# Kernel tuning notes

Hardware: AMD Instinct MI355X
Metric: run time of the kernel (lower is better)

Reference implementation:

```python
import jax, jax.numpy as jnp
import numpy as np

B, N, C_IN, C_OUT, K = 2, 8192, 128, 128, 21  # K = num_neighbors + 1 (self)
EPS = 1e-5

def knn_idx(xyz, k):
    # xyz: [B,N,3] -> idx [B,N,k] of k nearest neighbors (self included)
    d2 = jnp.sum(xyz * xyz, axis=-1)  # [B,N]
    dist = d2[:, :, None] + d2[:, None, :] - 2.0 * jnp.einsum('bnd,bmd->bnm', xyz, xyz)
    _, idx = jax.lax.top_k(-dist, k)
    return idx

def group_points(pts, idx):
    # pts [B,N,D], idx [B,N,K] -> [B,N,K,D]
    return jax.vmap(lambda p, i: p[i])(pts, idx)

def group_feats(f, idx):
    # f [B,C,N], idx [B,N,K] -> [B,C,N,K]
    return jax.vmap(lambda ff, i: ff[:, i])(f, idx)

def conv_bn_relu(x, W, g, b, m, v):
    # 1x1 conv (bias=False) + BatchNorm (inference stats) + ReLU
    y = jnp.einsum('oc,bcnk->bonk', W, x)
    inv = g / jnp.sqrt(v + EPS)
    return jax.nn.relu(y * inv[None, :, None, None] + (b - m * inv)[None, :, None, None])

def setup_inputs():
    key = jax.random.key(0)
    ks = jax.random.split(key, 12)
    return {
        'xyz': jax.random.normal(ks[0], (B, N, 3), jnp.float32),
        'f': jax.random.normal(ks[1], (B, C_IN, N), jnp.float32),
        'W_geo': jax.random.normal(ks[2], (C_OUT, 6), jnp.float32) * 0.1,
        'g_geo': jax.random.uniform(ks[3], (C_OUT,), jnp.float32, 0.5, 1.5),
        'b_geo': jax.random.normal(ks[4], (C_OUT,), jnp.float32) * 0.1,
        'm_geo': jax.random.normal(ks[5], (C_OUT,), jnp.float32) * 0.1,
        'v_geo': jax.random.uniform(ks[6], (C_OUT,), jnp.float32, 0.5, 1.5),
        'W_feat': jax.random.normal(ks[7], (C_OUT, 2 * C_IN), jnp.float32) * 0.05,
        'g_feat': jax.random.uniform(ks[8], (C_OUT,), jnp.float32, 0.5, 1.5),
        'b_feat': jax.random.normal(ks[9], (C_OUT,), jnp.float32) * 0.1,
        'm_feat': jax.random.normal(ks[10], (C_OUT,), jnp.float32) * 0.1,
        'v_feat': jax.random.uniform(ks[11], (C_OUT,), jnp.float32, 0.5, 1.5),
    }

def reference(xyz, f, W_geo, g_geo, b_geo, m_geo, v_geo, W_feat, g_feat, b_feat, m_feat, v_feat):
    idx = knn_idx(xyz, K)                                   # [B,N,K]
    grouped_xyz = group_points(xyz, idx)                    # [B,N,K,3]
    xyz_diff = jnp.transpose(grouped_xyz - xyz[:, :, None, :], (0, 3, 1, 2))  # [B,3,N,K]
    center = jnp.broadcast_to(jnp.transpose(xyz, (0, 2, 1))[:, :, :, None], (B, 3, N, K))
    G_geo = jnp.concatenate([center, xyz_diff], axis=1)     # [B,6,N,K]
    grouped_f = group_feats(f, idx)                         # [B,C,N,K]
    center_f = jnp.broadcast_to(f[:, :, :, None], (B, C_IN, N, K))
    G_feat = jnp.concatenate([center_f, grouped_f - center_f], axis=1)  # [B,2C,N,K]
    G_geo = conv_bn_relu(G_geo, W_geo, g_geo, b_geo, m_geo, v_geo)      # [B,C_OUT,N,K]
    G_feat = conv_bn_relu(G_feat, W_feat, g_feat, b_feat, m_feat, v_feat)
    feature = jnp.concatenate([G_geo, G_feat], axis=1)      # [B,2*C_OUT,N,K]
    return jnp.max(feature, axis=-1)                        # [B,2*C_OUT,N]
```

## Files before the change

### kernel.cpp

```cpp
#include <hip/hip_runtime.h>

typedef unsigned int u32;
typedef unsigned long long u64;
typedef unsigned short u16;

#define DEV __device__ __forceinline__

DEV u16 f2bf(float x) {
  u32 u = __float_as_uint(x);
  u32 r = u + 0x7fffu + ((u >> 16) & 1u);
  return (u16)(r >> 16);
}
DEV float bflo(u32 d) { return __uint_as_float(d << 16); }
DEV float bfhi(u32 d) { return __uint_as_float(d & 0xffff0000u); }
DEV u64 sortable64(double f) {
  long long b = __double_as_longlong(f);
  return (u64)b ^ (u64)((b >> 63) | (long long)0x8000000000000000ll);
}
DEV double ddist(double qx, double qy, double qz, double qd2,
                 float mxf, float myf, float mzf) {
  double cx = (double)mxf, cy = (double)myf, cz = (double)mzf;
  double cd2 = cx * cx + cy * cy + cz * cz;
  double dot = cx * qx + cy * qy + cz * qz;
  return (qd2 + cd2) - 2.0 * dot;
}

#define NB 2
#define NN 8192
#define NC 128
#define KK 21
#define MARGIN 1e-3f
#define CT 2048

__global__ __launch_bounds__(256) void k_prep(
    const float* __restrict__ Wf, const float* __restrict__ gf, const float* __restrict__ bf_,
    const float* __restrict__ mf, const float* __restrict__ vf,
    const float* __restrict__ Wg, const float* __restrict__ gg, const float* __restrict__ bg,
    const float* __restrict__ mg, const float* __restrict__ vg,
    u16* __restrict__ Wt, float* __restrict__ beta_f,
    float* __restrict__ Wgu, float* __restrict__ Wgv, float* __restrict__ beta_g) {
  int g = blockIdx.x * 256 + threadIdx.x;
  int c = g >> 8, o = g & 255;
  float val;
  if (o < 128) {
    float inv = gf[o] / sqrtf(vf[o] + 1e-5f);
    val = inv * (Wf[o * 256 + c] - Wf[o * 256 + c + 128]);
  } else {
    int o2 = o - 128;
    float inv = gf[o2] / sqrtf(vf[o2] + 1e-5f);
    val = inv * Wf[o2 * 256 + c + 128];
  }
  Wt[c * 256 + o] = f2bf(val);
  if (g < 128) {
    float inv = gf[g] / sqrtf(vf[g] + 1e-5f);
    beta_f[g] = bf_[g] - mf[g] * inv;
  } else if (g < 256) {
    int oo = g - 128;
    float invg = gg[oo] / sqrtf(vg[oo] + 1e-5f);
#pragma unroll
    for (int d = 0; d < 3; ++d) {
      Wgu[oo * 3 + d] = invg * (Wg[oo * 6 + d] - Wg[oo * 6 + 3 + d]);
      Wgv[oo * 3 + d] = invg * Wg[oo * 6 + 3 + d];
    }
    beta_g[oo] = bg[oo] - mg[oo] * invg;
  }
}

__global__ __launch_bounds__(256) void k_geo(
    const float* __restrict__ xyz, const float* __restrict__ Wgu, const float* __restrict__ Wgv,
    const float* __restrict__ beta_g, u32* __restrict__ ucat, u32* __restrict__ vcat) {
  int g = blockIdx.x * 256 + threadIdx.x;
  int p = g >> 6, oc = g & 63;
  const float* xp = xyz + p * 3;
  float X = xp[0], Y = xp[1], Z = xp[2];
  u32 du = 0, dv = 0;
#pragma unroll
  for (int h = 0; h < 2; ++h) {
    int o = oc * 2 + h;
    float ug = X * Wgu[o * 3] + Y * Wgu[o * 3 + 1] + Z * Wgu[o * 3 + 2] + beta_g[o];
    float vv = X * Wgv[o * 3] + Y * Wgv[o * 3 + 1] + Z * Wgv[o * 3 + 2];
    du |= (u32)f2bf(ug) << (16 * h);
    dv |= (u32)f2bf(vv) << (16 * h);
  }
  ucat[p * 128 + oc] = du;
  vcat[p * 128 + oc] = dv;
}

__global__ __launch_bounds__(256) void k_feat(
    const float* __restrict__ f, const u32* __restrict__ Wt32, const float* __restrict__ beta_f,
    u32* __restrict__ ucat, u32* __restrict__ vcat) {
  __shared__ u32 sW[128 * 128];
  __shared__ float sF[128][68];

  const int t = threadIdx.x;
  const int b = blockIdx.x >> 7;
  const int n0 = (blockIdx.x & 127) << 6;
  const int boff = b * (NC * NN);

#pragma unroll
  for (int k = 0; k < 64; ++k) sW[t + (k << 8)] = Wt32[t + (k << 8)];
#pragma unroll
  for (int k = 0; k < 32; ++k) {
    int i = t + (k << 8);
    int c = i >> 6, col = i & 63;
    sF[c][col] = f[boff + c * NN + n0 + col];
  }
  __syncthreads();

  const int w = t >> 6, lane = t & 63;
  const int og = lane >> 3, pg = lane & 7;
  const int o0 = w * 64 + og * 8;
  const int p0 = pg * 8;

  float acc[8][8];
#pragma unroll
  for (int a = 0; a < 8; ++a)
#pragma unroll
    for (int p = 0; p < 8; ++p) acc[a][p] = 0.0f;

  for (int c = 0; c < 128; ++c) {
    float4 fa = *(const float4*)&sF[c][p0];
    float4 fb = *(const float4*)&sF[c][p0 + 4];
    uint4 wr = *(const uint4*)&sW[c * 128 + (o0 >> 1)];
    float wv[8] = {bflo(wr.x), bfhi(wr.x), bflo(wr.y), bfhi(wr.y),
                   bflo(wr.z), bfhi(wr.z), bflo(wr.w), bfhi(wr.w)};
    float fv[8] = {fa.x, fa.y, fa.z, fa.w, fb.x, fb.y, fb.z, fb.w};
#pragma unroll
    for (int a = 0; a < 8; ++a)
#pragma unroll
      for (int p = 0; p < 8; ++p) acc[a][p] = __builtin_fmaf(wv[a], fv[p], acc[a][p]);
  }

  const int ochan = o0 & 127;
  const bool is_u = (o0 < 128);
  float bet[8];
#pragma unroll
  for (int a = 0; a < 8; ++a) bet[a] = is_u ? beta_f[ochan + a] : 0.0f;
  u32* dstbase = is_u ? ucat : vcat;
#pragma unroll
  for (int p = 0; p < 8; ++p) {
    int pt = (b << 13) + n0 + p0 + p;
    u32 d0 = (u32)f2bf(acc[0][p] + bet[0]) | ((u32)f2bf(acc[1][p] + bet[1]) << 16);
    u32 d1 = (u32)f2bf(acc[2][p] + bet[2]) | ((u32)f2bf(acc[3][p] + bet[3]) << 16);
    u32 d2 = (u32)f2bf(acc[4][p] + bet[4]) | ((u32)f2bf(acc[5][p] + bet[5]) << 16);
    u32 d3 = (u32)f2bf(acc[6][p] + bet[6]) | ((u32)f2bf(acc[7][p] + bet[7]) << 16);
    *(uint4*)&dstbase[pt * 128 + 64 + (ochan >> 1)] = make_uint4(d0, d1, d2, d3);
  }
}

__global__ __launch_bounds__(256, 4) void k_knn(const float* __restrict__ xyz,
                                                int* __restrict__ knn) {
  __shared__ float4 sc[CT];
  __shared__ u16 ssurv[16][128];
  __shared__ u32 scnt[16];

  const int t = threadIdx.x;
  const int blk = blockIdx.x;
  const int b = blk >> 9;
  const int n0 = (blk & 511) << 4;
  const float* X = xyz + b * (NN * 3);

  if (t < 16) scnt[t] = 0u;

  const int w = t >> 6, lane = t & 63;

  float mx[4], my[4], mz[4];
#pragma unroll
  for (int i = 0; i < 4; ++i) {
    int q = n0 + (w << 2) + i;
    mx[i] = -2.0f * X[q * 3];
    my[i] = -2.0f * X[q * 3 + 1];
    mz[i] = -2.0f * X[q * 3 + 2];
  }

  float mn[4];
#pragma unroll
  for (int i = 0; i < 4; ++i) mn[i] = __builtin_inff();

  for (int ct = 0; ct < NN / CT; ++ct) {
    __syncthreads();
    const float* Xt = X + ct * (CT * 3);
#pragma unroll
    for (int k = 0; k < 8; ++k) {
      int c = (k << 8) + t;
      float x = Xt[c * 3], y = Xt[c * 3 + 1], z = Xt[c * 3 + 2];
      float d2 = __builtin_fmaf(x, x, __builtin_fmaf(y, y, z * z));
      sc[c] = make_float4(x, y, z, d2);
    }
    __syncthreads();
#pragma unroll 4
    for (int cc = 0; cc < CT; cc += 64) {
      float4 C = sc[cc + lane];
#pragma unroll
      for (int i = 0; i < 4; ++i) {
        float s = __builtin_fmaf(C.x, mx[i],
                  __builtin_fmaf(C.y, my[i],
                  __builtin_fmaf(C.z, mz[i], C.w)));
        mn[i] = fminf(mn[i], s);
      }
    }
  }

  float thr[4];
#pragma unroll
  for (int i = 0; i < 4; ++i) {
    float v = mn[i];
#pragma unroll
    for (int k = 2; k <= 64; k <<= 1) {
#pragma unroll
      for (int j = k >> 1; j > 0; j >>= 1) {
        float p = __shfl_xor(v, j);
        bool takeMin = (((lane & k) == 0) == ((lane & j) == 0));
        v = takeMin ? fminf(v, p) : fmaxf(v, p);
      }
    }
    thr[i] = __shfl(v, 20) + MARGIN;
  }

  for (int ct = 0; ct < NN / CT; ++ct) {
    __syncthreads();
    const float* Xt = X + ct * (CT * 3);
#pragma unroll
    for (int k = 0; k < 8; ++k) {
      int c = (k << 8) + t;
      float x = Xt[c * 3], y = Xt[c * 3 + 1], z = Xt[c * 3 + 2];
      float d2 = __builtin_fmaf(x, x, __builtin_fmaf(y, y, z * z));
      sc[c] = make_float4(x, y, z, d2);
    }
    __syncthreads();
    int mbase = ct * CT + lane;
#pragma unroll 4
    for (int cc = 0; cc < CT; cc += 64) {
      float4 C = sc[cc + lane];
#pragma unroll
      for (int i = 0; i < 4; ++i) {
        float s = __builtin_fmaf(C.x, mx[i],
                  __builtin_fmaf(C.y, my[i],
                  __builtin_fmaf(C.z, mz[i], C.w)));
        if (s <= thr[i]) {
          int qq = (w << 2) + i;
          u32 slot = atomicAdd(&scnt[qq], 1u);
          if (slot < 128u) ssurv[qq][slot] = (u16)(mbase + cc);
        }
      }
    }
  }
  __syncthreads();

#pragma unroll 1
  for (int i = 0; i < 4; ++i) {
    const int qq = (w << 2) + i;
    const int q = n0 + qq;
    double Qx = (double)X[q * 3], Qy = (double)X[q * 3 + 1], Qz = (double)X[q * 3 + 2];
    double Qd2 = Qx * Qx + Qy * Qy + Qz * Qz;
    u32 cnt = scnt[qq];
    int* outp = knn + ((b << 13) + q) * KK;

    bool v0 = ((u32)lane < cnt);
    u32 m0 = v0 ? (u32)ssurv[qq][lane] : 0u;
    double s0 = ddist(Qx, Qy, Qz, Qd2, X[m0 * 3], X[m0 * 3 + 1], X[m0 * 3 + 2]);
    u64 k0 = v0 ? ((sortable64(s0) & 0xFFFFFFFFFFFFE000ull) | (u64)m0) : ~0ull;

    if (cnt <= 64u) {
      u64 v = k0;
#pragma unroll
      for (int k = 2; k <= 64; k <<= 1) {
#pragma unroll
        for (int j = k >> 1; j > 0; j >>= 1) {
          u64 p = __shfl_xor(v, j);
          bool takeMin = (((lane & k) == 0) == ((lane & j) == 0));
          bool pl = p < v;
          u64 mnv = pl ? p : v;
          u64 mxv = pl ? v : p;
          v = takeMin ? mnv : mxv;
        }
      }
      if (lane < KK) outp[lane] = (int)(v & 8191ull);
    } else {
      bool v1 = ((u32)(lane + 64) < cnt);
      u32 m1 = v1 ? (u32)ssurv[qq][lane + 64] : 0u;
      double s1 = ddist(Qx, Qy, Qz, Qd2, X[m1 * 3], X[m1 * 3 + 1], X[m1 * 3 + 2]);
      u64 k1 = v1 ? ((sortable64(s1) & 0xFFFFFFFFFFFFE000ull) | (u64)m1) : ~0ull;
      u32 selm = 0;
      for (int r = 0; r < KK; ++r) {
        u64 mk = (k0 < k1) ? k0 : k1;
#pragma unroll
        for (int j = 32; j > 0; j >>= 1) {
          u64 p = __shfl_xor(mk, j);
          if (p < mk) mk = p;
        }
        if (k0 == mk) k0 = ~0ull;
        else if (k1 == mk) k1 = ~0ull;
        if (lane == r) selm = (u32)(mk & 8191ull);
      }
      if (lane < KK) outp[lane] = (int)selm;
    }
  }
}

__global__ __launch_bounds__(256) void k_gather(
    const u32* __restrict__ ucat, const u32* __restrict__ vcat,
    const int* __restrict__ knn, float* __restrict__ out) {
  __shared__ float tr[64 * 258];

  const int t = threadIdx.x;
  const int b = blockIdx.x >> 7;
  const int n0 = (blockIdx.x & 127) << 6;
  const int w = t >> 6, lane = t & 63;
  const int which = w >> 1;
  const int lo = ((w & 1) << 6) | lane;

  for (int step = 0; step < 32; ++step) {
    int qq = step * 2 + which;
    int q = n0 + qq;
    const int* ip = knn + ((b << 13) + q) * KK;
    float a0 = -__builtin_inff(), a1 = -__builtin_inff();
#pragma unroll
    for (int k = 0; k < KK; ++k) {
      int p = ip[k];
      u32 d = vcat[(((b << 13) + p) << 7) + lo];
      a0 = fmaxf(a0, bflo(d));
      a1 = fmaxf(a1, bfhi(d));
    }
    u32 u = ucat[(((b << 13) + q) << 7) + lo];
    float r0 = fmaxf(bflo(u) + a0, 0.0f);
    float r1 = fmaxf(bfhi(u) + a1, 0.0f);
    *(float2*)&tr[qq * 258 + 2 * lo] = make_float2(r0, r1);
  }
  __syncthreads();

  float* ob = out + b * (256 * NN);
  for (int i = 0; i < 64; ++i) {
    int o = (w << 6) + i;
    ob[o * NN + n0 + lane] = tr[lane * 258 + o];
  }
}

extern "C" void kernel_launch(void* const* d_in, const int* in_sizes, int n_in,
                              void* d_out, int out_size, void* d_ws, size_t ws_size,
                              hipStream_t stream) {
  const float* xyz = (const float*)d_in[0];
  const float* f   = (const float*)d_in[1];
  const float* Wg  = (const float*)d_in[2];
  const float* gg  = (const float*)d_in[3];
  const float* bg  = (const float*)d_in[4];
  const float* mg  = (const float*)d_in[5];
  const float* vg  = (const float*)d_in[6];
  const float* Wf  = (const float*)d_in[7];
  const float* gf  = (const float*)d_in[8];
  const float* bf_ = (const float*)d_in[9];
  const float* mf  = (const float*)d_in[10];
  const float* vf  = (const float*)d_in[11];

  char* ws = (char*)d_ws;
  u16*   Wt     = (u16*)ws;
  float* beta_f = (float*)(ws + 65536);
  float* Wgu    = (float*)(ws + 66048);
  float* Wgv    = (float*)(ws + 67584);
  float* beta_g = (float*)(ws + 69120);
  u32*   ucat   = (u32*)(ws + 69632);
  u32*   vcat   = (u32*)(ws + 69632 + 8388608);
  int*   knn    = (int*)(ws + 69632 + 2 * 8388608);
  float* out    = (float*)d_out;

  if (ws_size < (size_t)(69632 + 2 * 8388608 + 16384 * KK * 4)) return;

  k_prep<<<dim3(128), dim3(256), 0, stream>>>(Wf, gf, bf_, mf, vf, Wg, gg, bg, mg, vg,
                                              Wt, beta_f, Wgu, Wgv, beta_g);
  k_geo<<<dim3(4096), dim3(256), 0, stream>>>(xyz, Wgu, Wgv, beta_g, ucat, vcat);
  k_feat<<<dim3(256), dim3(256), 0, stream>>>(f, (const u32*)Wt, beta_f, ucat, vcat);
  k_knn<<<dim3(1024), dim3(256), 0, stream>>>(xyz, knn);
  k_gather<<<dim3(256), dim3(256), 0, stream>>>(ucat, vcat, knn, out);
}
```

Baseline: 192.4 us.

## Restructure kNN distance scan with SoA tiles, 8 queries per wave, packed FMA

The kNN kernel stores candidate coordinates as separate x/y/z shared arrays filled through vectorized float4 global loads. Each pair of waves now covers 8 queries and splits the candidate tile in halves, so every shared load is reused across more queries. The distance math uses packed 2-wide FMAs and 3-input min, and the per-half thresholds are merged through shared memory. The squared norm is recomputed per candidate in registers and register pressure grows, and the survivor count is clamped to 128 before the final selection.

Result: slower. 200.3 us (+4.1%).

```diff
diff --git a/kernel.cpp b/kernel.cpp
--- a/kernel.cpp
+++ b/kernel.cpp
@@ -3,6 +3,7 @@
 typedef unsigned int u32;
 typedef unsigned long long u64;
 typedef unsigned short u16;
+typedef float v2f __attribute__((ext_vector_type(2)));
 
 #define DEV __device__ __forceinline__
 
@@ -24,6 +25,10 @@
   double dot = cx * qx + cy * qy + cz * qz;
   return (qd2 + cd2) - 2.0 * dot;
 }
+DEV float fmin3f(float a, float b, float c) {
+  return __builtin_fminf(__builtin_fminf(a, b), c);
+}
+DEV v2f vfma2(v2f a, v2f b, v2f c) { return __builtin_elementwise_fma(a, b, c); }
 
 #define NB 2
 #define NN 8192
@@ -150,9 +155,10 @@
 
 __global__ __launch_bounds__(256, 4) void k_knn(const float* __restrict__ xyz,
                                                 int* __restrict__ knn) {
-  __shared__ float4 sc[CT];
+  __shared__ float sx[CT], sy[CT], sz[CT];
   __shared__ u16 ssurv[16][128];
   __shared__ u32 scnt[16];
+  __shared__ float sthr[2][16];
 
   const int t = threadIdx.x;
   const int blk = blockIdx.x;
@@ -163,47 +169,62 @@
   if (t < 16) scnt[t] = 0u;
 
   const int w = t >> 6, lane = t & 63;
-
-  float mx[4], my[4], mz[4];
-#pragma unroll
-  for (int i = 0; i < 4; ++i) {
-    int q = n0 + (w << 2) + i;
+  const int g = w >> 1;
+  const int h = w & 1;
+  const int hb = h << 10;
+
+  float mx[8], my[8], mz[8];
+#pragma unroll
+  for (int i = 0; i < 8; ++i) {
+    int q = n0 + (g << 3) + i;
     mx[i] = -2.0f * X[q * 3];
     my[i] = -2.0f * X[q * 3 + 1];
     mz[i] = -2.0f * X[q * 3 + 2];
   }
 
-  float mn[4];
-#pragma unroll
-  for (int i = 0; i < 4; ++i) mn[i] = __builtin_inff();
+  float mn[8];
+#pragma unroll
+  for (int i = 0; i < 8; ++i) mn[i] = __builtin_inff();
 
   for (int ct = 0; ct < NN / CT; ++ct) {
     __syncthreads();
     const float* Xt = X + ct * (CT * 3);
 #pragma unroll
-    for (int k = 0; k < 8; ++k) {
-      int c = (k << 8) + t;
-      float x = Xt[c * 3], y = Xt[c * 3 + 1], z = Xt[c * 3 + 2];
-      float d2 = __builtin_fmaf(x, x, __builtin_fmaf(y, y, z * z));
-      sc[c] = make_float4(x, y, z, d2);
+    for (int g2 = 0; g2 < 2; ++g2) {
+      int c0 = (t << 2) + (g2 << 10);
+      const float* src = Xt + c0 * 3;
+      float4 q0 = *(const float4*)(src);
+      float4 q1 = *(const float4*)(src + 4);
+      float4 q2 = *(const float4*)(src + 8);
+      *(float4*)&sx[c0] = make_float4(q0.x, q0.w, q1.z, q2.y);
+      *(float4*)&sy[c0] = make_float4(q0.y, q1.x, q1.w, q2.z);
+      *(float4*)&sz[c0] = make_float4(q0.z, q1.y, q2.x, q2.w);
     }
     __syncthreads();
-#pragma unroll 4
-    for (int cc = 0; cc < CT; cc += 64) {
-      float4 C = sc[cc + lane];
-#pragma unroll
-      for (int i = 0; i < 4; ++i) {
-        float s = __builtin_fmaf(C.x, mx[i],
-                  __builtin_fmaf(C.y, my[i],
-                  __builtin_fmaf(C.z, mz[i], C.w)));
-        mn[i] = fminf(mn[i], s);
+#pragma unroll 2
+    for (int s8 = 0; s8 < 4; ++s8) {
+      int cb = hb + (s8 << 8) + (lane << 2);
+      float4 X4 = *(const float4*)&sx[cb];
+      float4 Y4 = *(const float4*)&sy[cb];
+      float4 Z4 = *(const float4*)&sz[cb];
+      v2f x01 = {X4.x, X4.y}, x23 = {X4.z, X4.w};
+      v2f y01 = {Y4.x, Y4.y}, y23 = {Y4.z, Y4.w};
+      v2f z01 = {Z4.x, Z4.y}, z23 = {Z4.z, Z4.w};
+      v2f w01 = vfma2(x01, x01, vfma2(y01, y01, z01 * z01));
+      v2f w23 = vfma2(x23, x23, vfma2(y23, y23, z23 * z23));
+#pragma unroll
+      for (int i = 0; i < 8; ++i) {
+        v2f mxv = {mx[i], mx[i]}, myv = {my[i], my[i]}, mzv = {mz[i], mz[i]};
+        v2f s01 = vfma2(x01, mxv, vfma2(y01, myv, vfma2(z01, mzv, w01)));
+        v2f s23 = vfma2(x23, mxv, vfma2(y23, myv, vfma2(z23, mzv, w23)));
+        mn[i] = fmin3f(mn[i], s01.x, s01.y);
+        mn[i] = fmin3f(mn[i], s23.x, s23.y);
       }
     }
   }
 
-  float thr[4];
-#pragma unroll
-  for (int i = 0; i < 4; ++i) {
+#pragma unroll 1
+  for (int i = 0; i < 8; ++i) {
     float v = mn[i];
 #pragma unroll
     for (int k = 2; k <= 64; k <<= 1) {
@@ -214,33 +235,65 @@
         v = takeMin ? fminf(v, p) : fmaxf(v, p);
       }
     }
-    thr[i] = __shfl(v, 20) + MARGIN;
+    float tw = __shfl(v, 20);
+    if (lane == 0) sthr[h][(g << 3) + i] = tw;
+  }
+  __syncthreads();
+  float thr[8];
+#pragma unroll
+  for (int i = 0; i < 8; ++i) {
+    int qq = (g << 3) + i;
+    thr[i] = fminf(sthr[0][qq], sthr[1][qq]) + MARGIN;
   }
 
   for (int ct = 0; ct < NN / CT; ++ct) {
     __syncthreads();
     const float* Xt = X + ct * (CT * 3);
 #pragma unroll
-    for (int k = 0; k < 8; ++k) {
-      int c = (k << 8) + t;
-      float x = Xt[c * 3], y = Xt[c * 3 + 1], z = Xt[c * 3 + 2];
-      float d2 = __builtin_fmaf(x, x, __builtin_fmaf(y, y, z * z));
-      sc[c] = make_float4(x, y, z, d2);
+    for (int g2 = 0; g2 < 2; ++g2) {
+      int c0 = (t << 2) + (g2 << 10);
+      const float* src = Xt + c0 * 3;
+      float4 q0 = *(const float4*)(src);
+      float4 q1 = *(const float4*)(src + 4);
+      float4 q2 = *(const float4*)(src + 8);
+      *(float4*)&sx[c0] = make_float4(q0.x, q0.w, q1.z, q2.y);
+      *(float4*)&sy[c0] = make_float4(q0.y, q1.x, q1.w, q2.z);
+      *(float4*)&sz[c0] = make_float4(q0.z, q1.y, q2.x, q2.w);
     }
     __syncthreads();
-    int mbase = ct * CT + lane;
-#pragma unroll 4
-    for (int cc = 0; cc < CT; cc += 64) {
-      float4 C = sc[cc + lane];
-#pragma unroll
-      for (int i = 0; i < 4; ++i) {
-        float s = __builtin_fmaf(C.x, mx[i],
-                  __builtin_fmaf(C.y, my[i],
-                  __builtin_fmaf(C.z, mz[i], C.w)));
-        if (s <= thr[i]) {
-          int qq = (w << 2) + i;
+#pragma unroll 1
+    for (int s8 = 0; s8 < 4; ++s8) {
+      int cb = hb + (s8 << 8) + (lane << 2);
+      float4 X4 = *(const float4*)&sx[cb];
+      float4 Y4 = *(const float4*)&sy[cb];
+      float4 Z4 = *(const float4*)&sz[cb];
+      v2f x01 = {X4.x, X4.y}, x23 = {X4.z, X4.w};
+      v2f y01 = {Y4.x, Y4.y}, y23 = {Y4.z, Y4.w};
+      v2f z01 = {Z4.x, Z4.y}, z23 = {Z4.z, Z4.w};
+      v2f w01 = vfma2(x01, x01, vfma2(y01, y01, z01 * z01));
+      v2f w23 = vfma2(x23, x23, vfma2(y23, y23, z23 * z23));
+      int mbase = ct * CT + cb;
+#pragma unroll
+      for (int i = 0; i < 8; ++i) {
+        v2f mxv = {mx[i], mx[i]}, myv = {my[i], my[i]}, mzv = {mz[i], mz[i]};
+        v2f s01 = vfma2(x01, mxv, vfma2(y01, myv, vfma2(z01, mzv, w01)));
+        v2f s23 = vfma2(x23, mxv, vfma2(y23, myv, vfma2(z23, mzv, w23)));
+        int qq = (g << 3) + i;
+        if (s01.x <= thr[i]) {
           u32 slot = atomicAdd(&scnt[qq], 1u);
-          if (slot < 128u) ssurv[qq][slot] = (u16)(mbase + cc);
+          if (slot < 128u) ssurv[qq][slot] = (u16)(mbase + 0);
+        }
+        if (s01.y <= thr[i]) {
+          u32 slot = atomicAdd(&scnt[qq], 1u);
+          if (slot < 128u) ssurv[qq][slot] = (u16)(mbase + 1);
+        }
+        if (s23.x <= thr[i]) {
+          u32 slot = atomicAdd(&scnt[qq], 1u);
+          if (slot < 128u) ssurv[qq][slot] = (u16)(mbase + 2);
+        }
+        if (s23.y <= thr[i]) {
+          u32 slot = atomicAdd(&scnt[qq], 1u);
+          if (slot < 128u) ssurv[qq][slot] = (u16)(mbase + 3);
         }
       }
     }
@@ -254,6 +307,7 @@
     double Qx = (double)X[q * 3], Qy = (double)X[q * 3 + 1], Qz = (double)X[q * 3 + 2];
     double Qd2 = Qx * Qx + Qy * Qy + Qz * Qz;
     u32 cnt = scnt[qq];
+    if (cnt > 128u) cnt = 128u;
     int* outp = knn + ((b << 13) + q) * KK;
 
     bool v0 = ((u32)lane < cnt);
```
